# Kernel tuning notes

Measured on AMD Instinct MI355X. Metric: run time of the kernel, lower is better.

Reference implementation:

```python
import jax, jax.numpy as jnp
import numpy as np

N = 207      # node_size (METR-LA)
E = 1722     # edge_size from edge CSV
RES = 12     # resolution
T = 288 // RES  # time-of-day slots


def setup_inputs() -> dict:
    key = jax.random.key(0)
    ks = jax.random.split(key, 12)
    B, L = 64, 2048
    return {
        "inputs": jax.random.normal(ks[0], (B, 2, N, L), jnp.float32),
        "ind": jax.random.randint(ks[1], (B,), 0, 288),
        "edge_from": jax.random.randint(ks[2], (E,), 0, N),
        "edge_to": jax.random.randint(ks[3], (E,), 0, N),
        "weight_react": jax.random.normal(ks[4], (T, E), jnp.float32) / 10.0,
        "weight_diff": jax.random.normal(ks[5], (T, E), jnp.float32) / 1000.0,
        "weight_react_a": jax.random.normal(ks[6], (T, E), jnp.float32) / 10.0,
        "weight_diff_a": jax.random.normal(ks[7], (T, E), jnp.float32) / 1000.0,
        "bias_reaction": jax.random.normal(ks[8], (T, N), jnp.float32) / 10.0,
        "bias_diffusion": jax.random.normal(ks[9], (T, N), jnp.float32) / 10.0,
        "bias_reaction_a": jax.random.normal(ks[10], (T, N), jnp.float32) / 10.0,
        "bias_diffusion_a": jax.random.normal(ks[11], (T, N), jnp.float32) / 10.0,
    }


def _scatter(w, src, dst):
    # dense NxN from edge list; duplicate edges accumulate (torch sparse coalesce semantics)
    return jnp.zeros((N, N), w.dtype).at[src, dst].add(w)


def _diag_colsum(A):
    # torch.sum(A, 1) on [1,N,N] sums over the first node axis -> column sums
    return jax.vmap(jnp.diag)(A.sum(axis=1))


def reference(inputs, ind, edge_from, edge_to,
              weight_react, weight_diff, weight_react_a, weight_diff_a,
              bias_reaction, bias_diffusion, bias_reaction_a, bias_diffusion_a):
    x = inputs[:, 0, :, :]              # [B, N, L]
    ii = ind // RES                      # [B] time-slot indices

    scat = jax.vmap(_scatter, in_axes=(0, None, None))
    Ar = scat(weight_react[ii], edge_from, edge_to)      # [B,N,N] index = (i, j)
    Ad = scat(weight_diff[ii], edge_to, edge_from)       # index_a = (j, i)
    Ara = scat(weight_react_a[ii], edge_from, edge_to)
    Ada = scat(weight_diff_a[ii], edge_to, edge_from)

    RW = _diag_colsum(Ar) - Ar           # Laplacian: D - A
    DW = _diag_colsum(Ad) - Ad
    RWa = _diag_colsum(Ara) + Ara        # D + A
    # faithful replication: batch element 0 uses diag of colsums of the already-built
    # reaction Laplacian (I1 - A) instead of reaction_weight_a (original-code quirk)
    RWa = RWa.at[0].set(jnp.diag(RW[0].sum(axis=0)) + Ara[0])
    DWa = _diag_colsum(Ada) + Ada

    conv = lambda A: jnp.einsum('nvl,nwv->nwl', x, A)   # out[n,w,l] = sum_v A[n,w,v] x[n,v,l]
    reaction = conv(RW) + bias_reaction[ii][:, :, None]
    reaction_a = conv(RWa) + bias_reaction_a[ii][:, :, None]
    diffusion = conv(DW) + bias_diffusion[ii][:, :, None]
    diffusion_a = conv(DWa) + bias_diffusion_a[ii][:, :, None]

    return jnp.tanh(reaction) + jnp.tanh(reaction_a) + diffusion + diffusion_a + x
```

## Files before the change

kernel.cpp:

```cpp
#include <hip/hip_runtime.h>
#include <cstdint>
#include <cstddef>

#define NN 207
#define NE 1722
#define NT 24
#define LL 2048
#define LCC 128
#define KP  224
#define KS  228
#define MTILES 13
#define KTILES 7


typedef float   f32x4 __attribute__((ext_vector_type(4)));
typedef _Float16 half8 __attribute__((ext_vector_type(8)));

__device__ __forceinline__ unsigned short f2h(float f) {
    return __builtin_bit_cast(unsigned short, (_Float16)f);
}
__device__ __forceinline__ float tanhfast(float z) {
    return 1.0f - __fdividef(2.0f, __expf(2.0f * z) + 1.0f);
}

__global__ void k_build(const int* __restrict__ efrom, const int* __restrict__ eto,
                        const float* __restrict__ wr, const float* __restrict__ wd,
                        const float* __restrict__ wra, const float* __restrict__ wda,
                        const float* __restrict__ br, const float* __restrict__ bd,
                        const float* __restrict__ bra, const float* __restrict__ bda,
                        unsigned short* __restrict__ Wpack,
                        float4* __restrict__ cb4, float4* __restrict__ bb4) {
    const int t   = blockIdx.x / MTILES;
    const int mt  = blockIdx.x % MTILES;
    const int tid = threadIdx.x;
    __shared__ float rowbuf[3][16][KP];
    __shared__ float cs[4][16];

    float* rb = &rowbuf[0][0][0];
    for (int i = tid; i < 3 * 16 * KP; i += 256) rb[i] = 0.0f;
    if (tid < 64) ((float*)cs)[tid] = 0.0f;
    __syncthreads();

    const int mt16 = mt * 16;
    const float* wrt  = wr  + (size_t)t * NE;
    const float* wdt  = wd  + (size_t)t * NE;
    const float* wrat = wra + (size_t)t * NE;
    const float* wdat = wda + (size_t)t * NE;
    for (int e = tid; e < NE; e += 256) {
        int ef = efrom[e], et = eto[e];
        unsigned rf = (unsigned)(ef - mt16), rt = (unsigned)(et - mt16);
        bool in_f = rf < 16u, in_t = rt < 16u;
        if (in_f || in_t) {
            float w1 = wrt[e], w2 = wdt[e], w3 = wrat[e], w4 = wdat[e];
            if (in_t) {
                atomicAdd(&rowbuf[2][rt][ef], w4 - w2);
                atomicAdd(&cs[0][rt], w1);
                atomicAdd(&cs[1][rt], w3);
            }
            if (in_f) {
                atomicAdd(&rowbuf[0][rf][et], -w1);
                atomicAdd(&rowbuf[1][rf][et],  w3);
                atomicAdd(&cs[2][rf], w2);
                atomicAdd(&cs[3][rf], w4);
            }
        }
    }
    __syncthreads();

    if (tid < 16) {
        int w = mt16 + tid;
        if (w < NN) {
            cb4[t * NN + w] = make_float4(cs[0][tid], cs[1][tid], cs[2][tid] + cs[3][tid], 0.0f);
            bb4[t * NN + w] = make_float4(br[t * NN + w], bra[t * NN + w],
                                          bd[t * NN + w] + bda[t * NN + w], 0.0f);
        }
    }

    for (int fr = tid; fr < 3 * KTILES * 64; fr += 256) {
        int mat = fr / (KTILES * 64);
        int rem = fr - mat * (KTILES * 64);
        int ks = rem >> 6, l = rem & 63;
        int r = l & 15, g = l >> 4;
        const float* src = &rowbuf[mat][r][0];
        unsigned short h[8];
        #pragma unroll
        for (int e2 = 0; e2 < 4; ++e2) h[e2]     = f2h(src[ks * 32 + 4 * g + e2]);
        #pragma unroll
        for (int e2 = 0; e2 < 4; ++e2) h[4 + e2] = f2h(src[ks * 32 + 16 + 4 * g + e2]);
        uint4 pv;
        pv.x = (unsigned)h[0] | ((unsigned)h[1] << 16);
        pv.y = (unsigned)h[2] | ((unsigned)h[3] << 16);
        pv.z = (unsigned)h[4] | ((unsigned)h[5] << 16);
        pv.w = (unsigned)h[6] | ((unsigned)h[7] << 16);
        size_t o = ((size_t)(((t * MTILES + mt) * 3 + mat) * KTILES + ks) * 64 + l) * 8;
        *(uint4*)(Wpack + o) = pv;
    }
}

__global__ __launch_bounds__(512, 4) void k_mfma(
    const float* __restrict__ inputs, const int* __restrict__ ind,
    const unsigned short* __restrict__ Wpack,
    const float4* __restrict__ cb4, const float4* __restrict__ bb4,
    float* __restrict__ out) {
    __shared__ unsigned short xT[LCC * KS];
    __shared__ float4 lcb[NN], lbb[NN];
    const int b = blockIdx.y, chunk = blockIdx.x, tid = threadIdx.x;
    const int t = ind[b] / 12;

    for (int i = tid; i < NN; i += 512) { lcb[i] = cb4[t * NN + i]; lbb[i] = bb4[t * NN + i]; }
    {
        int4 z = make_int4(0, 0, 0, 0);
        for (int i = tid; i < LCC * KS * 2 / 16; i += 512) ((int4*)xT)[i] = z;
    }
    __syncthreads();

    const float* xb = inputs + (size_t)b * (2 * NN * LL) + (size_t)chunk * LCC;
    for (int i = tid; i < NN * (LCC / 4); i += 512) {
        int k = i >> 5;
        int c4 = (i & 31) << 2;
        float4 v = *(const float4*)(xb + (size_t)k * LL + c4);
        xT[(c4 + 0) * KS + k] = f2h(v.x);
        xT[(c4 + 1) * KS + k] = f2h(v.y);
        xT[(c4 + 2) * KS + k] = f2h(v.z);
        xT[(c4 + 3) * KS + k] = f2h(v.w);
    }
    __syncthreads();

    const int l  = tid & 63, wv = tid >> 6;
    const int r  = l & 15,  g  = l >> 4;
    const int col = wv * 16 + r;

    half8 bf[KTILES];
    #pragma unroll
    for (int ks = 0; ks < KTILES; ++ks) {
        uint2 lo = *(const uint2*)&xT[col * KS + ks * 32 + 4 * g];
        uint2 hi = *(const uint2*)&xT[col * KS + ks * 32 + 16 + 4 * g];
        uint4 u; u.x = lo.x; u.y = lo.y; u.z = hi.x; u.w = hi.y;
        bf[ks] = __builtin_bit_cast(half8, u);
    }

    const unsigned short* Ap = Wpack + (size_t)t * (MTILES * 3 * KTILES * 512) + (size_t)l * 8;
    const float* xrd = inputs + (size_t)b * (2 * NN * LL) + (size_t)chunk * LCC + col;
    float* ob = out + (size_t)b * ((size_t)NN * LL) + (size_t)chunk * LCC + col;

    for (int mt = 0; mt < MTILES; ++mt) {
        f32x4 aR = {0.f, 0.f, 0.f, 0.f};
        f32x4 aA = {0.f, 0.f, 0.f, 0.f};
        f32x4 aD = {0.f, 0.f, 0.f, 0.f};
        #pragma unroll
        for (int ks = 0; ks < KTILES; ++ks) {
            half8 a = __builtin_bit_cast(half8, *(const uint4*)Ap); Ap += 512;
            aR = __builtin_amdgcn_mfma_f32_16x16x32_f16(a, bf[ks], aR, 0, 0, 0);
        }
        #pragma unroll
        for (int ks = 0; ks < KTILES; ++ks) {
            half8 a = __builtin_bit_cast(half8, *(const uint4*)Ap); Ap += 512;
            aA = __builtin_amdgcn_mfma_f32_16x16x32_f16(a, bf[ks], aA, 0, 0, 0);
        }
        #pragma unroll
        for (int ks = 0; ks < KTILES; ++ks) {
            half8 a = __builtin_bit_cast(half8, *(const uint4*)Ap); Ap += 512;
            aD = __builtin_amdgcn_mfma_f32_16x16x32_f16(a, bf[ks], aD, 0, 0, 0);
        }
        const int rowb = mt * 16 + 4 * g;
        #pragma unroll
        for (int q = 0; q < 4; ++q) {
            int row = rowb + q;
            if (row < NN) {
                float xq = xrd[(size_t)row * LL];
                float4 cb = lcb[row], bb = lbb[row];
                float rr = aR[q] + cb.x * xq + bb.x;
                float ra = aA[q] + bb.y;
                if (b != 0) ra += cb.y * xq;
                float dd = aD[q] + cb.z * xq + bb.z;
                ob[(size_t)row * LL] = tanhfast(rr) + tanhfast(ra) + dd + xq;
            }
        }
    }
}

extern "C" void kernel_launch(void* const* d_in, const int* in_sizes, int n_in,
                              void* d_out, int out_size, void* d_ws, size_t ws_size,
                              hipStream_t stream) {
    const float* inputs = (const float*)d_in[0];
    const int*   ind    = (const int*)d_in[1];
    const int*   efrom  = (const int*)d_in[2];
    const int*   eto    = (const int*)d_in[3];
    const float* wr     = (const float*)d_in[4];
    const float* wd     = (const float*)d_in[5];
    const float* wra    = (const float*)d_in[6];
    const float* wda    = (const float*)d_in[7];
    const float* br     = (const float*)d_in[8];
    const float* bd     = (const float*)d_in[9];
    const float* bra    = (const float*)d_in[10];
    const float* bda    = (const float*)d_in[11];
    float* out = (float*)d_out;

    char* ws = (char*)d_ws;
    float4*         cb4   = (float4*)(ws + 0);
    float4*         bb4   = (float4*)(ws + 79488);
    unsigned short* Wpack = (unsigned short*)(ws + 158976);

    const int B = in_sizes[1];

    k_build<<<dim3(NT * MTILES), dim3(256), 0, stream>>>(
        efrom, eto, wr, wd, wra, wda, br, bd, bra, bda, Wpack, cb4, bb4);
    k_mfma<<<dim3(LL / LCC, B), dim3(512), 0, stream>>>(
        inputs, ind, Wpack, cb4, bb4, out);
}
```

Measured before the change: 418.7 us.

## Use swizzled row-major fp16 LDS tile and shrink LDS footprint for occupancy

Stores the input chunk in LDS row-major with an XOR swizzle and packed ushort4 writes, instead of the transposed layout built from scalar 2-byte scatters. It also trims the K padding to 208, drops the full LDS zeroing pass and one barrier, and reads the per-row coefficients straight from global memory. The residual x is now read back from the fp16 LDS copy rather than from global, and the occupancy hint is raised. The smaller LDS footprint should let more blocks share a CU. The cost is more scalar LDS reads when gathering B fragments, and the residual term loses precision because it now goes through fp16.

Result: slower. 457.2 us (+9.2%).

```diff
diff --git a/kernel.cpp b/kernel.cpp
--- a/kernel.cpp
+++ b/kernel.cpp
@@ -7,13 +7,14 @@
 #define NT 24
 #define LL 2048
 #define LCC 128
-#define KP  224
-#define KS  228
+#define KP  208
 #define MTILES 13
 #define KTILES 7
-
-
-typedef float   f32x4 __attribute__((ext_vector_type(4)));
+#define CH_U16 3584
+#define T_U16 (MTILES * 3 * CH_U16)
+
+
+typedef float    f32x4 __attribute__((ext_vector_type(4)));
 typedef _Float16 half8 __attribute__((ext_vector_type(8)));
 
 __device__ __forceinline__ unsigned short f2h(float f) {
@@ -79,68 +80,79 @@
     for (int fr = tid; fr < 3 * KTILES * 64; fr += 256) {
         int mat = fr / (KTILES * 64);
         int rem = fr - mat * (KTILES * 64);
-        int ks = rem >> 6, l = rem & 63;
-        int r = l & 15, g = l >> 4;
+        int ks = rem >> 6, lq = rem & 63;
+        int r = lq & 15, g = lq >> 4;
         const float* src = &rowbuf[mat][r][0];
+        int k0 = ks * 32 + 4 * g;
         unsigned short h[8];
         #pragma unroll
-        for (int e2 = 0; e2 < 4; ++e2) h[e2]     = f2h(src[ks * 32 + 4 * g + e2]);
-        #pragma unroll
-        for (int e2 = 0; e2 < 4; ++e2) h[4 + e2] = f2h(src[ks * 32 + 16 + 4 * g + e2]);
+        for (int e2 = 0; e2 < 4; ++e2) {
+            h[e2] = f2h(src[k0 + e2]);
+            int kb = k0 + 16 + e2;
+            h[4 + e2] = (kb < KP) ? f2h(src[kb]) : (unsigned short)0;
+        }
         uint4 pv;
         pv.x = (unsigned)h[0] | ((unsigned)h[1] << 16);
         pv.y = (unsigned)h[2] | ((unsigned)h[3] << 16);
         pv.z = (unsigned)h[4] | ((unsigned)h[5] << 16);
         pv.w = (unsigned)h[6] | ((unsigned)h[7] << 16);
-        size_t o = ((size_t)(((t * MTILES + mt) * 3 + mat) * KTILES + ks) * 64 + l) * 8;
+        size_t o = ((size_t)(t * MTILES + mt) * 3 + mat) * CH_U16 + (size_t)ks * 512 + (size_t)lq * 8;
         *(uint4*)(Wpack + o) = pv;
     }
 }
 
-__global__ __launch_bounds__(512, 4) void k_mfma(
+__global__ __launch_bounds__(512, 6) void k_mfma(
     const float* __restrict__ inputs, const int* __restrict__ ind,
     const unsigned short* __restrict__ Wpack,
     const float4* __restrict__ cb4, const float4* __restrict__ bb4,
     float* __restrict__ out) {
-    __shared__ unsigned short xT[LCC * KS];
-    __shared__ float4 lcb[NN], lbb[NN];
+    __shared__ unsigned short xs[KP * LCC];
     const int b = blockIdx.y, chunk = blockIdx.x, tid = threadIdx.x;
     const int t = ind[b] / 12;
 
-    for (int i = tid; i < NN; i += 512) { lcb[i] = cb4[t * NN + i]; lbb[i] = bb4[t * NN + i]; }
-    {
-        int4 z = make_int4(0, 0, 0, 0);
-        for (int i = tid; i < LCC * KS * 2 / 16; i += 512) ((int4*)xT)[i] = z;
-    }
-    __syncthreads();
+    if (tid < 64) ((unsigned*)(xs + 207 * LCC))[tid] = 0u;
 
     const float* xb = inputs + (size_t)b * (2 * NN * LL) + (size_t)chunk * LCC;
-    for (int i = tid; i < NN * (LCC / 4); i += 512) {
-        int k = i >> 5;
+    for (int i = tid; i < 207 * 32; i += 512) {
+        int k  = i >> 5;
         int c4 = (i & 31) << 2;
         float4 v = *(const float4*)(xb + (size_t)k * LL + c4);
-        xT[(c4 + 0) * KS + k] = f2h(v.x);
-        xT[(c4 + 1) * KS + k] = f2h(v.y);
-        xT[(c4 + 2) * KS + k] = f2h(v.z);
-        xT[(c4 + 3) * KS + k] = f2h(v.w);
+        int gk = (k >> 2) & 3;
+        ushort4 h;
+        h.x = f2h(v.x); h.y = f2h(v.y); h.z = f2h(v.z); h.w = f2h(v.w);
+        *(ushort4*)&xs[k * LCC + (c4 ^ (gk << 3))] = h;
     }
     __syncthreads();
 
     const int l  = tid & 63, wv = tid >> 6;
     const int r  = l & 15,  g  = l >> 4;
-    const int col = wv * 16 + r;
+    const int col  = wv * 16 + r;
+    const int colx = col ^ (g << 3);
+    const _Float16* xh = (const _Float16*)xs;
 
     half8 bf[KTILES];
     #pragma unroll
-    for (int ks = 0; ks < KTILES; ++ks) {
-        uint2 lo = *(const uint2*)&xT[col * KS + ks * 32 + 4 * g];
-        uint2 hi = *(const uint2*)&xT[col * KS + ks * 32 + 16 + 4 * g];
-        uint4 u; u.x = lo.x; u.y = lo.y; u.z = hi.x; u.w = hi.y;
-        bf[ks] = __builtin_bit_cast(half8, u);
-    }
-
-    const unsigned short* Ap = Wpack + (size_t)t * (MTILES * 3 * KTILES * 512) + (size_t)l * 8;
-    const float* xrd = inputs + (size_t)b * (2 * NN * LL) + (size_t)chunk * LCC + col;
+    for (int ks = 0; ks < KTILES - 1; ++ks) {
+        half8 v;
+        int k0 = ks * 32 + 4 * g;
+        #pragma unroll
+        for (int e = 0; e < 4; ++e) {
+            v[e]     = xh[(k0 + e) * LCC + colx];
+            v[4 + e] = xh[(k0 + 16 + e) * LCC + colx];
+        }
+        bf[ks] = v;
+    }
+    {
+        half8 v = {0, 0, 0, 0, 0, 0, 0, 0};
+        int k0 = 192 + 4 * g;
+        #pragma unroll
+        for (int e = 0; e < 4; ++e) v[e] = xh[(k0 + e) * LCC + colx];
+        bf[KTILES - 1] = v;
+    }
+
+    const unsigned short* Ap = Wpack + (size_t)t * T_U16 + (size_t)l * 8;
+    const float4* cbp = cb4 + (size_t)t * NN;
+    const float4* bbp = bb4 + (size_t)t * NN;
     float* ob = out + (size_t)b * ((size_t)NN * LL) + (size_t)chunk * LCC + col;
 
     for (int mt = 0; mt < MTILES; ++mt) {
@@ -149,26 +161,28 @@
         f32x4 aD = {0.f, 0.f, 0.f, 0.f};
         #pragma unroll
         for (int ks = 0; ks < KTILES; ++ks) {
-            half8 a = __builtin_bit_cast(half8, *(const uint4*)Ap); Ap += 512;
+            half8 a = __builtin_bit_cast(half8, *(const uint4*)(Ap + ks * 512));
             aR = __builtin_amdgcn_mfma_f32_16x16x32_f16(a, bf[ks], aR, 0, 0, 0);
         }
         #pragma unroll
         for (int ks = 0; ks < KTILES; ++ks) {
-            half8 a = __builtin_bit_cast(half8, *(const uint4*)Ap); Ap += 512;
+            half8 a = __builtin_bit_cast(half8, *(const uint4*)(Ap + CH_U16 + ks * 512));
             aA = __builtin_amdgcn_mfma_f32_16x16x32_f16(a, bf[ks], aA, 0, 0, 0);
         }
         #pragma unroll
         for (int ks = 0; ks < KTILES; ++ks) {
-            half8 a = __builtin_bit_cast(half8, *(const uint4*)Ap); Ap += 512;
+            half8 a = __builtin_bit_cast(half8, *(const uint4*)(Ap + 2 * CH_U16 + ks * 512));
             aD = __builtin_amdgcn_mfma_f32_16x16x32_f16(a, bf[ks], aD, 0, 0, 0);
         }
+        Ap += 3 * CH_U16;
+
         const int rowb = mt * 16 + 4 * g;
         #pragma unroll
         for (int q = 0; q < 4; ++q) {
             int row = rowb + q;
             if (row < NN) {
-                float xq = xrd[(size_t)row * LL];
-                float4 cb = lcb[row], bb = lbb[row];
+                float xq = (float)xh[row * LCC + colx];
+                float4 cb = cbp[row], bb = bbp[row];
                 float rr = aR[q] + cb.x * xq + bb.x;
                 float ra = aA[q] + bb.y;
                 if (b != 0) ra += cb.y * xq;
```
